# Optimization experiments

Measured on AMD Instinct MI355X. Metric: run time of the kernel, lower is better.

## Reference

```python
import jax, jax.numpy as jnp
import numpy as np
import math

EMBED_DIM = 1024
NUM_HEADS = 16
HEAD_DIM = EMBED_DIM // NUM_HEADS
SEQ = 1024
BATCH = 8


def setup_inputs() -> dict:
    key = jax.random.key(0)
    k1, k2, k3, k4, k5 = jax.random.split(key, 5)
    q = jax.random.normal(k1, (SEQ, BATCH, EMBED_DIM), dtype=jnp.float32)
    # module asserts key == query (self-attention only)
    in_proj_w = jax.random.normal(k2, (3 * EMBED_DIM, EMBED_DIM), dtype=jnp.float32) * 0.02
    in_proj_b = jax.random.normal(k3, (3 * EMBED_DIM,), dtype=jnp.float32) * 0.02
    out_proj_w = jax.random.normal(k4, (EMBED_DIM, EMBED_DIM), dtype=jnp.float32) * 0.02
    out_proj_b = jax.random.normal(k5, (EMBED_DIM,), dtype=jnp.float32) * 0.02
    return {
        "query": q,
        "key": q,
        "value": q,
        "in_proj_w": in_proj_w,
        "in_proj_b": in_proj_b,
        "out_proj_w": out_proj_w,
        "out_proj_b": out_proj_b,
    }


def reference(query, key, value, in_proj_w, in_proj_b, out_proj_w, out_proj_b):
    s, b, e = query.shape
    nh, hd = NUM_HEADS, HEAD_DIM
    norm = math.sqrt(hd)
    # fused QKV projection: [s, b, 3e]
    mixed = query @ in_proj_w.T + in_proj_b
    mixed = mixed.reshape(s, b, nh, 3 * hd)
    q, k, v = jnp.split(mixed, 3, axis=-1)  # each [s, b, nh, hd]
    # -> [b*nh, s, hd]
    q = q.reshape(s, b * nh, hd).transpose(1, 0, 2) / norm
    k = k.reshape(s, b * nh, hd).transpose(1, 0, 2)
    v = v.reshape(s, b * nh, hd).transpose(1, 0, 2)
    # full O(s^2) attention matrix, as in the original bmm/softmax/bmm
    scores = jnp.einsum('nqd,nkd->nqk', q, k)  # [b*nh, s, s]
    probs = jax.nn.softmax(scores, axis=-1)
    ctx = jnp.einsum('nqk,nkd->nqd', probs, v)  # [b*nh, s, hd]
    # [b*nh, s, hd] -> [s, b, e]
    ctx = ctx.reshape(b, nh, s, hd).transpose(2, 0, 1, 3).reshape(s, b, e)
    return ctx @ out_proj_w.T + out_proj_b
```

## Files before the change

kernel.cpp:

```cpp
#include <hip/hip_runtime.h>

typedef __bf16 bf16_t;
typedef __bf16 bf16x8 __attribute__((ext_vector_type(8)));
typedef float f32x4 __attribute__((ext_vector_type(4)));

#define MFMA16(a, b, c) __builtin_amdgcn_mfma_f32_16x16x32_bf16((a), (b), (c), 0, 0, 0)

__device__ __forceinline__ const bf16_t* tile_ptr(const bf16_t* t, int row, int kchunk) {
    return t + row * 64 + (((kchunk ^ (row & 7))) << 3);
}

__device__ __forceinline__ void stage64(const bf16_t* __restrict__ gbase, size_t gstride,
                                        bf16_t* lds_rowbase, int lane) {
    const int rr = lane >> 3, cl = lane & 7;
    const bf16_t* g = gbase + (size_t)rr * gstride + ((cl ^ rr) << 3);
    __builtin_amdgcn_global_load_lds((__attribute__((address_space(1))) const void*)g,
                                     (__attribute__((address_space(3))) void*)lds_rowbase,
                                     16, 0, 0);
}

__device__ __forceinline__ int cs_addr(int m, int n) {
    return m * 128 + ((((n >> 3) ^ ((m >> 3) & 7))) << 3) + (n & 7);
}

__global__ void __launch_bounds__(256) k_cvt(
    const float* __restrict__ q, const float* __restrict__ wi, const float* __restrict__ wo,
    bf16_t* __restrict__ qb, bf16_t* __restrict__ wib, bf16_t* __restrict__ wob)
{
    const int g = blockIdx.x * 256 + threadIdx.x;
    const float* src; bf16_t* dst; int off;
    if (g < 1048576)      { src = q;  dst = qb;  off = g; }
    else if (g < 1441792) { src = wi; dst = wib; off = g - 1048576; }
    else                  { src = wo; dst = wob; off = g - 1441792; }
    const float4* s4 = (const float4*)(src + (size_t)off * 8);
    float4 a = s4[0], b = s4[1];
    bf16x8 v;
    v[0] = (bf16_t)a.x; v[1] = (bf16_t)a.y; v[2] = (bf16_t)a.z; v[3] = (bf16_t)a.w;
    v[4] = (bf16_t)b.x; v[5] = (bf16_t)b.y; v[6] = (bf16_t)b.z; v[7] = (bf16_t)b.w;
    *(bf16x8*)(dst + (size_t)off * 8) = v;
}

__global__ void __launch_bounds__(256) k_qkv(
    const bf16_t* __restrict__ A, const bf16_t* __restrict__ W,
    const float* __restrict__ bias,
    bf16_t* __restrict__ Qh, bf16_t* __restrict__ Kh, bf16_t* __restrict__ Vt)
{
    __shared__ bf16_t smem[16384];
    bf16_t* As = smem;
    bf16_t* Bs = smem + 8192;
    const int m0 = blockIdx.x * 128;
    const int n0 = blockIdx.y * 128;
    const int which = n0 >> 10;
    const int hbase = (n0 & 1023) >> 6;
    const int t = threadIdx.x;
    const int wave = t >> 6, lane = t & 63;
    const int quad = lane >> 4, l16 = lane & 15;
    const int wm = (wave & 1) * 64, wn = (wave >> 1) * 64;

    f32x4 acc[4][4] = {};

    for (int k0 = 0; k0 < 1024; k0 += 64) {
        __syncthreads();
        #pragma unroll
        for (int p = 0; p < 4; ++p) {
            const int rb = wave * 32 + p * 8;
            stage64(A + (size_t)(m0 + rb) * 1024 + k0, 1024, As + rb * 64, lane);
            const int np = n0 + rb;
            const int wrow = ((np & 1023) >> 6) * 192 + which * 64 + (np & 63);
            stage64(W + (size_t)wrow * 1024 + k0, 1024, Bs + rb * 64, lane);
        }
        __syncthreads();
        #pragma unroll
        for (int ks = 0; ks < 2; ++ks) {
            bf16x8 af[4], bf[4];
            #pragma unroll
            for (int i = 0; i < 4; ++i)
                af[i] = *(const bf16x8*)tile_ptr(As, wm + i * 16 + l16, ks * 4 + quad);
            #pragma unroll
            for (int j = 0; j < 4; ++j)
                bf[j] = *(const bf16x8*)tile_ptr(Bs, wn + j * 16 + l16, ks * 4 + quad);
            #pragma unroll
            for (int i = 0; i < 4; ++i)
                #pragma unroll
                for (int j = 0; j < 4; ++j)
                    acc[i][j] = MFMA16(af[i], bf[j], acc[i][j]);
        }
    }

    __syncthreads();
    const float scale = (which == 0) ? 0.125f : 1.0f;
    #pragma unroll
    for (int j = 0; j < 4; ++j) {
        const int nl = wn + j * 16 + l16;
        const float bv = bias[(hbase + (nl >> 6)) * 192 + which * 64 + (nl & 63)];
        #pragma unroll
        for (int i = 0; i < 4; ++i) {
            #pragma unroll
            for (int rg = 0; rg < 4; ++rg) {
                const int ml = wm + i * 16 + quad * 4 + rg;
                smem[cs_addr(ml, nl)] = (bf16_t)((acc[i][j][rg] + bv) * scale);
            }
        }
    }
    __syncthreads();

    const int si0 = m0 >> 3;
    if (which < 2) {
        bf16_t* dst = which ? Kh : Qh;
        #pragma unroll
        for (int u = 0; u < 4; ++u) {
            const int unit = wave * 4 + u;
            const int h = unit >> 3, bi = unit & 7;
            const int head = bi * 16 + hbase + h;
            #pragma unroll
            for (int pass = 0; pass < 2; ++pass) {
                const int si = pass * 8 + (lane >> 3);
                const int dc = lane & 7;
                const int ml = si * 8 + bi;
                const int nch = (h * 8 + dc) ^ (si & 7);
                bf16x8 v = *(const bf16x8*)&smem[ml * 128 + nch * 8];
                *(bf16x8*)(dst + (size_t)head * 65536 + (size_t)(si0 + si) * 64 + dc * 8) = v;
            }
        }
    } else {
        #pragma unroll
        for (int u = 0; u < 8; ++u) {
            const int unit = wave * 8 + u;
            const int h = unit >> 4, bi = (unit >> 1) & 7, c = unit & 1;
            const int head = bi * 16 + hbase + h;
            const int d = lane;
            bf16x8 v;
            #pragma unroll
            for (int e = 0; e < 8; ++e) {
                const int ml = (c * 8 + e) * 8 + bi;
                const int nch = (h * 8 + (d >> 3)) ^ e;
                v[e] = smem[ml * 128 + nch * 8 + (d & 7)];
            }
            *(bf16x8*)(Vt + (size_t)head * 65536 +
                       (size_t)(si0 / 8 + c) * 512 + (size_t)d * 8) = v;
        }
    }
}

__global__ void __launch_bounds__(256) k_attn(
    const bf16_t* __restrict__ Qh, const bf16_t* __restrict__ Kh,
    const bf16_t* __restrict__ Vg, bf16_t* __restrict__ Ctx)
{
    __shared__ bf16_t Qs[128 * 64];
    __shared__ bf16_t Ks[64 * 64];
    __shared__ bf16_t Vts[80 * 64];
    __shared__ bf16_t Ps[4][32][72];

    const int head = blockIdx.x >> 3;
    const int qt = blockIdx.x & 7;
    const int t = threadIdx.x;
    const int wave = t >> 6, lane = t & 63;
    const int quad = lane >> 4, l16 = lane & 15;

    const bf16_t* Qg = Qh + (size_t)head * 65536 + (size_t)qt * 8192;
    const bf16_t* Kg = Kh + (size_t)head * 65536;
    const bf16_t* Vgh = Vg + (size_t)head * 65536;

    #pragma unroll
    for (int p = 0; p < 4; ++p) {
        const int rb = wave * 32 + p * 8;
        stage64(Qg + (size_t)rb * 64, 64, Qs + rb * 64, lane);
    }
    #pragma unroll
    for (int i = 0; i < 4; ++i) {
        const int idx = t * 4 + i;
        Vts[64 * 64 + idx] = (bf16_t)((idx < 64) ? 1.0f : 0.0f);
    }
    __syncthreads();

    bf16x8 qf[2][2];
    #pragma unroll
    for (int half = 0; half < 2; ++half)
        #pragma unroll
        for (int ks = 0; ks < 2; ++ks)
            qf[half][ks] = *(const bf16x8*)tile_ptr(Qs, wave * 32 + half * 16 + l16, ks * 4 + quad);

    bf16x8 vf_ones[2];
    #pragma unroll
    for (int ks = 0; ks < 2; ++ks)
        vf_ones[ks] = *(const bf16x8*)tile_ptr(Vts, 64 + l16, ks * 4 + quad);

    f32x4 vacc[2][5] = {};

    for (int kt = 0; kt < 16; ++kt) {
        __syncthreads();
        #pragma unroll
        for (int p = 0; p < 2; ++p) {
            const int rb = wave * 16 + p * 8;
            stage64(Kg + (size_t)(kt * 64 + rb) * 64, 64, Ks + rb * 64, lane);
            {
                const int rr = lane >> 3, cl = lane & 7;
                const bf16_t* g = Vgh + (size_t)(kt * 8 + (cl ^ rr)) * 512
                                      + (size_t)(rb + rr) * 8;
                __builtin_amdgcn_global_load_lds(
                    (__attribute__((address_space(1))) const void*)g,
                    (__attribute__((address_space(3))) void*)(Vts + rb * 64), 16, 0, 0);
            }
        }
        __syncthreads();

        f32x4 s[2][4] = {};
        #pragma unroll
        for (int ks = 0; ks < 2; ++ks) {
            #pragma unroll
            for (int j = 0; j < 4; ++j) {
                bf16x8 kf = *(const bf16x8*)tile_ptr(Ks, j * 16 + l16, ks * 4 + quad);
                s[0][j] = MFMA16(qf[0][ks], kf, s[0][j]);
                s[1][j] = MFMA16(qf[1][ks], kf, s[1][j]);
            }
        }

        #pragma unroll
        for (int half = 0; half < 2; ++half)
            #pragma unroll
            for (int j = 0; j < 4; ++j)
                #pragma unroll
                for (int rg = 0; rg < 4; ++rg)
                    Ps[wave][half * 16 + quad * 4 + rg][j * 16 + l16] =
                        (bf16_t)exp2f(s[half][j][rg] * 1.44269504088896f);
        asm volatile("s_waitcnt lgkmcnt(0)" ::: "memory");

        #pragma unroll
        for (int ks = 0; ks < 2; ++ks) {
            bf16x8 pf0 = *(const bf16x8*)&Ps[wave][l16][ks * 32 + quad * 8];
            bf16x8 pf1 = *(const bf16x8*)&Ps[wave][16 + l16][ks * 32 + quad * 8];
            #pragma unroll
            for (int n = 0; n < 4; ++n) {
                bf16x8 vf = *(const bf16x8*)tile_ptr(Vts, n * 16 + l16, ks * 4 + quad);
                vacc[0][n] = MFMA16(pf0, vf, vacc[0][n]);
                vacc[1][n] = MFMA16(pf1, vf, vacc[1][n]);
            }
            vacc[0][4] = MFMA16(pf0, vf_ones[ks], vacc[0][4]);
            vacc[1][4] = MFMA16(pf1, vf_ones[ks], vacc[1][4]);
        }
    }

    const int bi = head >> 4, h = head & 15;
    #pragma unroll
    for (int half = 0; half < 2; ++half) {
        #pragma unroll
        for (int rg = 0; rg < 4; ++rg) {
            const float l = __shfl(vacc[half][4][rg], lane & 48, 64);
            const float inv = 1.0f / l;
            const int si = qt * 128 + wave * 32 + half * 16 + quad * 4 + rg;
            #pragma unroll
            for (int n = 0; n < 4; ++n)
                Ctx[((size_t)si * 8 + bi) * 1024 + h * 64 + n * 16 + l16] =
                    (bf16_t)(vacc[half][n][rg] * inv);
        }
    }
}

__global__ void __launch_bounds__(256) k_out(
    const bf16_t* __restrict__ A, const bf16_t* __restrict__ W,
    const float* __restrict__ bias, float* __restrict__ out)
{
    __shared__ bf16_t As[128 * 64];
    __shared__ bf16_t Bs[128 * 64];
    const int m0 = blockIdx.x * 128;
    const int n0 = blockIdx.y * 128;
    const int t = threadIdx.x;
    const int wave = t >> 6, lane = t & 63;
    const int quad = lane >> 4, l16 = lane & 15;
    const int wm = (wave & 1) * 64, wn = (wave >> 1) * 64;

    f32x4 acc[4][4] = {};

    for (int k0 = 0; k0 < 1024; k0 += 64) {
        __syncthreads();
        #pragma unroll
        for (int p = 0; p < 4; ++p) {
            const int rb = wave * 32 + p * 8;
            stage64(A + (size_t)(m0 + rb) * 1024 + k0, 1024, As + rb * 64, lane);
            stage64(W + (size_t)(n0 + rb) * 1024 + k0, 1024, Bs + rb * 64, lane);
        }
        __syncthreads();
        #pragma unroll
        for (int ks = 0; ks < 2; ++ks) {
            bf16x8 af[4], bf[4];
            #pragma unroll
            for (int i = 0; i < 4; ++i)
                af[i] = *(const bf16x8*)tile_ptr(As, wm + i * 16 + l16, ks * 4 + quad);
            #pragma unroll
            for (int j = 0; j < 4; ++j)
                bf[j] = *(const bf16x8*)tile_ptr(Bs, wn + j * 16 + l16, ks * 4 + quad);
            #pragma unroll
            for (int i = 0; i < 4; ++i)
                #pragma unroll
                for (int j = 0; j < 4; ++j)
                    acc[i][j] = MFMA16(af[i], bf[j], acc[i][j]);
        }
    }

    #pragma unroll
    for (int j = 0; j < 4; ++j) {
        const int n = n0 + wn + j * 16 + l16;
        const float bv = bias[n];
        #pragma unroll
        for (int i = 0; i < 4; ++i) {
            #pragma unroll
            for (int rg = 0; rg < 4; ++rg) {
                const int m = m0 + wm + i * 16 + quad * 4 + rg;
                out[(size_t)m * 1024 + n] = acc[i][j][rg] + bv;
            }
        }
    }
}

extern "C" void kernel_launch(void* const* d_in, const int* in_sizes, int n_in,
                              void* d_out, int out_size, void* d_ws, size_t ws_size,
                              hipStream_t stream)
{
    const float* query = (const float*)d_in[0];
    const float* in_w  = (const float*)d_in[3];
    const float* in_b  = (const float*)d_in[4];
    const float* out_w = (const float*)d_in[5];
    const float* out_b = (const float*)d_in[6];
    float* out = (float*)d_out;

    bf16_t* Wi  = (bf16_t*)d_ws;
    bf16_t* Wo  = Wi + (size_t)3145728;
    bf16_t* Qh  = Wo + (size_t)1048576;
    bf16_t* Kh  = Qh + (size_t)8388608;
    bf16_t* Vt  = Kh + (size_t)8388608;
    bf16_t* Aq  = Vt + (size_t)8388608;
    bf16_t* Ctx = Aq;

    k_cvt<<<dim3(6144), 256, 0, stream>>>(query, in_w, out_w, Aq, Wi, Wo);
    k_qkv<<<dim3(64, 24), 256, 0, stream>>>(Aq, Wi, in_b, Qh, Kh, Vt);
    k_attn<<<dim3(1024), 256, 0, stream>>>(Qh, Kh, Vt, Ctx);
    k_out<<<dim3(64, 8), 256, 0, stream>>>(Ctx, Wo, out_b, out);
}
```

Before: 310.0 us.

## Restructure attention kernel: transposed S, swizzled P, direct Q loads, head-interleaved grid

Folds the log2(e) factor into the Q scale so the softmax exp needs no extra multiply. Swaps the MFMA operands so each lane holds a row of S, letting P be written as packed 4-wide bf16 stores into an XOR-swizzled LDS tile. Q fragments are loaded straight from global memory instead of being staged through LDS. The ones vector for the row-sum is built in registers, the block-to-head mapping is reordered to interleave heads, and launch bounds request 4 blocks per CU. Together these cut LDS use and bank conflicts and aim for higher occupancy, at the cost of uncoalesced Q loads and possible register pressure.

```diff
diff --git a/kernel.cpp b/kernel.cpp
--- a/kernel.cpp
+++ b/kernel.cpp
@@ -1,6 +1,7 @@
 #include <hip/hip_runtime.h>
 
 typedef __bf16 bf16_t;
+typedef __bf16 bf16x4 __attribute__((ext_vector_type(4)));
 typedef __bf16 bf16x8 __attribute__((ext_vector_type(8)));
 typedef float f32x4 __attribute__((ext_vector_type(4)));
 
@@ -88,7 +89,7 @@
     }
 
     __syncthreads();
-    const float scale = (which == 0) ? 0.125f : 1.0f;
+    const float scale = (which == 0) ? 0.180336880111112f : 1.0f;
     #pragma unroll
     for (int j = 0; j < 4; ++j) {
         const int nl = wn + j * 16 + l16;
@@ -142,17 +143,17 @@
     }
 }
 
-__global__ void __launch_bounds__(256) k_attn(
+__global__ void __launch_bounds__(256, 4) k_attn(
     const bf16_t* __restrict__ Qh, const bf16_t* __restrict__ Kh,
     const bf16_t* __restrict__ Vg, bf16_t* __restrict__ Ctx)
 {
-    __shared__ bf16_t Qs[128 * 64];
     __shared__ bf16_t Ks[64 * 64];
-    __shared__ bf16_t Vts[80 * 64];
-    __shared__ bf16_t Ps[4][32][72];
-
-    const int head = blockIdx.x >> 3;
-    const int qt = blockIdx.x & 7;
+    __shared__ bf16_t Vts[64 * 64];
+    __shared__ bf16_t Pw[4][32 * 64];
+
+    const int bid = blockIdx.x;
+    const int head = (bid & 7) * 16 + ((bid >> 3) & 15);
+    const int qt = bid >> 7;
     const int t = threadIdx.x;
     const int wave = t >> 6, lane = t & 63;
     const int quad = lane >> 4, l16 = lane & 15;
@@ -161,29 +162,17 @@
     const bf16_t* Kg = Kh + (size_t)head * 65536;
     const bf16_t* Vgh = Vg + (size_t)head * 65536;
 
-    #pragma unroll
-    for (int p = 0; p < 4; ++p) {
-        const int rb = wave * 32 + p * 8;
-        stage64(Qg + (size_t)rb * 64, 64, Qs + rb * 64, lane);
-    }
-    #pragma unroll
-    for (int i = 0; i < 4; ++i) {
-        const int idx = t * 4 + i;
-        Vts[64 * 64 + idx] = (bf16_t)((idx < 64) ? 1.0f : 0.0f);
-    }
-    __syncthreads();
-
     bf16x8 qf[2][2];
     #pragma unroll
     for (int half = 0; half < 2; ++half)
         #pragma unroll
         for (int ks = 0; ks < 2; ++ks)
-            qf[half][ks] = *(const bf16x8*)tile_ptr(Qs, wave * 32 + half * 16 + l16, ks * 4 + quad);
-
-    bf16x8 vf_ones[2];
-    #pragma unroll
-    for (int ks = 0; ks < 2; ++ks)
-        vf_ones[ks] = *(const bf16x8*)tile_ptr(Vts, 64 + l16, ks * 4 + quad);
+            qf[half][ks] = *(const bf16x8*)(
+                Qg + (size_t)(wave * 32 + half * 16 + l16) * 64 + ks * 32 + quad * 8);
+
+    bf16x8 ones;
+    #pragma unroll
+    for (int e = 0; e < 8; ++e) ones[e] = (bf16_t)((l16 == 0) ? 1.0f : 0.0f);
 
     f32x4 vacc[2][5] = {};
 
@@ -210,33 +199,38 @@
             #pragma unroll
             for (int j = 0; j < 4; ++j) {
                 bf16x8 kf = *(const bf16x8*)tile_ptr(Ks, j * 16 + l16, ks * 4 + quad);
-                s[0][j] = MFMA16(qf[0][ks], kf, s[0][j]);
-                s[1][j] = MFMA16(qf[1][ks], kf, s[1][j]);
-            }
-        }
-
-        #pragma unroll
-        for (int half = 0; half < 2; ++half)
-            #pragma unroll
-            for (int j = 0; j < 4; ++j)
+                s[0][j] = MFMA16(kf, qf[0][ks], s[0][j]);
+                s[1][j] = MFMA16(kf, qf[1][ks], s[1][j]);
+            }
+        }
+
+        #pragma unroll
+        for (int half = 0; half < 2; ++half) {
+            const int row = half * 16 + l16;
+            #pragma unroll
+            for (int j = 0; j < 4; ++j) {
+                bf16x4 pv;
                 #pragma unroll
                 for (int rg = 0; rg < 4; ++rg)
-                    Ps[wave][half * 16 + quad * 4 + rg][j * 16 + l16] =
-                        (bf16_t)exp2f(s[half][j][rg] * 1.44269504088896f);
+                    pv[rg] = (bf16_t)exp2f(s[half][j][rg]);
+                const int chunk = j * 2 + (quad >> 1);
+                *(bf16x4*)&Pw[wave][row * 64 + ((chunk ^ (row & 7)) << 3) + (quad & 1) * 4] = pv;
+            }
+        }
         asm volatile("s_waitcnt lgkmcnt(0)" ::: "memory");
 
         #pragma unroll
         for (int ks = 0; ks < 2; ++ks) {
-            bf16x8 pf0 = *(const bf16x8*)&Ps[wave][l16][ks * 32 + quad * 8];
-            bf16x8 pf1 = *(const bf16x8*)&Ps[wave][16 + l16][ks * 32 + quad * 8];
+            bf16x8 pf0 = *(const bf16x8*)tile_ptr(Pw[wave], l16, ks * 4 + quad);
+            bf16x8 pf1 = *(const bf16x8*)tile_ptr(Pw[wave], 16 + l16, ks * 4 + quad);
             #pragma unroll
             for (int n = 0; n < 4; ++n) {
                 bf16x8 vf = *(const bf16x8*)tile_ptr(Vts, n * 16 + l16, ks * 4 + quad);
                 vacc[0][n] = MFMA16(pf0, vf, vacc[0][n]);
                 vacc[1][n] = MFMA16(pf1, vf, vacc[1][n]);
             }
-            vacc[0][4] = MFMA16(pf0, vf_ones[ks], vacc[0][4]);
-            vacc[1][4] = MFMA16(pf1, vf_ones[ks], vacc[1][4]);
+            vacc[0][4] = MFMA16(pf0, ones, vacc[0][4]);
+            vacc[1][4] = MFMA16(pf1, ones, vacc[1][4]);
         }
     }
 
```

Result: faster. 276.3 us (-10.9%).
